# Performance work log

Hardware: AMD Instinct MI355X
Metric: run time of the kernel (lower is better)

The kernel has to match this reference:

```python
import jax, jax.numpy as jnp
import numpy as np

N_FEAT = 256
N_HID = 128
N_HEAD = 4
N_HEAD_LAST = 6
N_CLASS = 40
NEG_SLOPE = 0.2


def gat_conv(x, src, dst, W, att_src, att_dst, bias, heads, ch, concat):
    # x: [N, in], W: [in, heads*ch], att_*: [heads, ch]
    N = x.shape[0]
    xw = (x @ W).reshape(N, heads, ch)                      # [N, H, C]
    a_src = jnp.sum(xw * att_src, axis=-1)                  # [N, H]
    a_dst = jnp.sum(xw * att_dst, axis=-1)                  # [N, H]
    e = jax.nn.leaky_relu(a_src[src] + a_dst[dst], NEG_SLOPE)  # [E, H]
    # softmax over incoming edges of each destination node
    m = jax.ops.segment_max(e, dst, num_segments=N)         # [N, H]
    ex = jnp.exp(e - m[dst])
    denom = jax.ops.segment_sum(ex, dst, num_segments=N)    # [N, H]
    alpha = ex / (denom[dst] + 1e-16)                       # [E, H]
    msg = xw[src] * alpha[..., None]                        # [E, H, C]
    out = jax.ops.segment_sum(msg, dst, num_segments=N)     # [N, H, C]
    out = out.reshape(N, heads * ch) if concat else out.mean(axis=1)
    return out + bias


def setup_inputs() -> dict:
    key = jax.random.key(0)
    ks = jax.random.split(key, 16)
    N, E = 10000, 160000
    x = jax.random.normal(ks[0], (N, N_FEAT), dtype=jnp.float32)
    edge_index = jax.random.randint(ks[1], (2, E), 0, N, dtype=jnp.int64)
    hid = N_HID * N_HEAD  # 512
    s = lambda fan: 1.0 / np.sqrt(fan)
    return {
        "x": x,
        "edge_index": edge_index,
        "W0": jax.random.normal(ks[2], (N_FEAT, hid), jnp.float32) * s(N_FEAT),
        "a_src0": jax.random.normal(ks[3], (N_HEAD, N_HID), jnp.float32) * s(N_HID),
        "a_dst0": jax.random.normal(ks[4], (N_HEAD, N_HID), jnp.float32) * s(N_HID),
        "b0": jnp.zeros((hid,), jnp.float32),
        "Wskip_in": jax.random.normal(ks[5], (N_FEAT, hid), jnp.float32) * s(N_FEAT),
        "W1": jax.random.normal(ks[6], (hid, hid), jnp.float32) * s(hid),
        "a_src1": jax.random.normal(ks[7], (N_HEAD, N_HID), jnp.float32) * s(N_HID),
        "a_dst1": jax.random.normal(ks[8], (N_HEAD, N_HID), jnp.float32) * s(N_HID),
        "b1": jnp.zeros((hid,), jnp.float32),
        "W2": jax.random.normal(ks[9], (hid, N_HEAD_LAST * N_CLASS), jnp.float32) * s(hid),
        "a_src2": jax.random.normal(ks[10], (N_HEAD_LAST, N_CLASS), jnp.float32) * s(N_CLASS),
        "a_dst2": jax.random.normal(ks[11], (N_HEAD_LAST, N_CLASS), jnp.float32) * s(N_CLASS),
        "b2": jnp.zeros((N_CLASS,), jnp.float32),
        "Wskip_out": jax.random.normal(ks[12], (hid, N_CLASS), jnp.float32) * s(hid),
    }


def reference(x, edge_index, W0, a_src0, a_dst0, b0, Wskip_in,
              W1, a_src1, a_dst1, b1,
              W2, a_src2, a_dst2, b2, Wskip_out):
    N = x.shape[0]
    loops = jnp.arange(N, dtype=edge_index.dtype)
    src = jnp.concatenate([edge_index[0], loops])  # add self loops (PyG GATConv)
    dst = jnp.concatenate([edge_index[1], loops])
    # eval mode: dropout is identity
    h = gat_conv(x, src, dst, W0, a_src0, a_dst0, b0, N_HEAD, N_HID, True)
    x1 = jax.nn.elu(h + x @ Wskip_in)                      # res skip w/ projection
    h = gat_conv(x1, src, dst, W1, a_src1, a_dst1, b1, N_HEAD, N_HID, True)
    x2 = jax.nn.elu(h + x1)                                # res skip, same dims
    h = gat_conv(x2, src, dst, W2, a_src2, a_dst2, b2, N_HEAD_LAST, N_CLASS, False)
    out = h + x2 @ Wskip_out                               # out_skip 'res'
    return out
```

## Files before the change

kernel.cpp:

```cpp
#include <hip/hip_runtime.h>
#include <math.h>


#define N_FEAT 256
#define HID 512

using u16 = unsigned short;
using bf16x8 = __attribute__((ext_vector_type(8))) __bf16;
using f32x16 = __attribute__((ext_vector_type(16))) float;

__device__ inline u16 bf16_rne(float f) {
    unsigned u = __float_as_uint(f);
    return (u16)((u + 0x7fffu + ((u >> 16) & 1u)) >> 16);
}
__device__ inline float bf16_to_f32(u16 h) {
    return __uint_as_float((unsigned)h << 16);
}
__device__ inline bf16x8 ldb8(const u16* p) {
    return *reinterpret_cast<const bf16x8*>(p);
}


__global__ void init_counts(int* cursor, int N) {
    int i = blockIdx.x * blockDim.x + threadIdx.x;
    if (i < N) cursor[i] = 1;
}

__global__ void count_edges(const int* __restrict__ ei, int E, int* cursor) {
    int e = blockIdx.x * blockDim.x + threadIdx.x;
    if (e < E) atomicAdd(&cursor[ei[E + e]], 1);
}

__global__ __launch_bounds__(1024) void scan_offsets(int* cursor, int* row_off, int N) {
    __shared__ int sdata[1024];
    int tid = threadIdx.x;
    int chunk = (N + 1023) >> 10;
    int base = tid * chunk;
    int lsum = 0;
    for (int i = 0; i < chunk; i++) {
        int idx = base + i;
        if (idx < N) lsum += cursor[idx];
    }
    sdata[tid] = lsum;
    __syncthreads();
    for (int off = 1; off < 1024; off <<= 1) {
        int t = (tid >= off) ? sdata[tid - off] : 0;
        __syncthreads();
        sdata[tid] += t;
        __syncthreads();
    }
    int run = sdata[tid] - lsum;
    if (tid == 0) row_off[0] = 0;
    for (int i = 0; i < chunk; i++) {
        int idx = base + i;
        if (idx < N) {
            int c = cursor[idx];
            cursor[idx] = run;
            run += c;
            row_off[idx + 1] = run;
        }
    }
}

__global__ void fill_csr(const int* __restrict__ ei, int E, int N,
                         int* cursor, int* __restrict__ col) {
    int i = blockIdx.x * blockDim.x + threadIdx.x;
    int tot = E + N;
    if (i >= tot) return;
    int s, d;
    if (i < E) { s = ei[i]; d = ei[E + i]; }
    else       { s = i - E; d = s; }
    int pos = atomicAdd(&cursor[d], 1);
    col[pos] = s;
}


__global__ __launch_bounds__(256) void att_combine_all(
        const float* __restrict__ W0, const float* __restrict__ as0, const float* __restrict__ ad0,
        const float* __restrict__ W1, const float* __restrict__ as1, const float* __restrict__ ad1,
        const float* __restrict__ W2, const float* __restrict__ as2, const float* __restrict__ ad2,
        float* __restrict__ ac0, float* __restrict__ ac1, float* __restrict__ ac2) {
    int i = blockIdx.x * blockDim.x + threadIdx.x;
    const float *W, *as_, *ad_;
    float* ac;
    int K, H, C, li;
    if (i < 2048)       { W = W0; as_ = as0; ad_ = ad0; ac = ac0; K = 256; H = 4; C = 128; li = i; }
    else if (i < 6144)  { W = W1; as_ = as1; ad_ = ad1; ac = ac1; K = 512; H = 4; C = 128; li = i - 2048; }
    else if (i < 12288) { W = W2; as_ = as2; ad_ = ad2; ac = ac2; K = 512; H = 6; C = 40;  li = i - 6144; }
    else return;
    int k = li / (2 * H);
    int hh = li - k * 2 * H;
    int h = (hh >= H) ? hh - H : hh;
    const float* av = ((hh >= H) ? ad_ : as_) + h * C;
    const float* wp = W + (size_t)k * H * C + (size_t)h * C;
    float sum = 0.f;
    for (int c = 0; c < C; c++) sum = fmaf(wp[c], av[c], sum);
    ac[(size_t)k * 2 * H + hh] = sum;
}


__global__ __launch_bounds__(256) void cvtA_pack(const float* __restrict__ X,
                                                 u16* __restrict__ hi, u16* __restrict__ lo,
                                                 int M, int K, int Rblocks) {
    int gid = blockIdx.x * blockDim.x + threadIdx.x;
    int lane = gid & 63;
    int rest = gid >> 6;
    int KC = K >> 4;
    int R = rest / KC;
    int c = rest - R * KC;
    if (R >= Rblocks) return;
    int row = R * 32 + (lane & 31);
    if (row >= M) row = M - 1;
    const float* src = X + (size_t)row * K + c * 16 + (lane >> 5) * 8;
    float4 v0 = *reinterpret_cast<const float4*>(src);
    float4 v1 = *reinterpret_cast<const float4*>(src + 4);
    float vv[8] = {v0.x, v0.y, v0.z, v0.w, v1.x, v1.y, v1.z, v1.w};
    unsigned hp[4], lp[4];
    #pragma unroll
    for (int j = 0; j < 4; j++) {
        u16 h0 = bf16_rne(vv[2 * j]);
        u16 h1 = bf16_rne(vv[2 * j + 1]);
        float r0 = vv[2 * j]     - __uint_as_float((unsigned)h0 << 16);
        float r1 = vv[2 * j + 1] - __uint_as_float((unsigned)h1 << 16);
        u16 l0 = bf16_rne(r0);
        u16 l1 = bf16_rne(r1);
        hp[j] = (unsigned)h0 | ((unsigned)h1 << 16);
        lp[j] = (unsigned)l0 | ((unsigned)l1 << 16);
    }
    size_t dst = ((size_t)rest * 64 + lane) * 8;
    *reinterpret_cast<int4*>(hi + dst) = make_int4(hp[0], hp[1], hp[2], hp[3]);
    *reinterpret_cast<int4*>(lo + dst) = make_int4(lp[0], lp[1], lp[2], lp[3]);
}

__device__ inline void cvtB_body(const float* __restrict__ B,
                                 u16* __restrict__ hi, u16* __restrict__ lo,
                                 int K, int Nb, int gid) {
    int lane = gid & 63;
    int rest = gid >> 6;
    int KC = K >> 4;
    int Cb = rest / KC;
    int c = rest - Cb * KC;
    int n = Cb * 32 + (lane & 31);
    int kbase = c * 16 + (lane >> 5) * 8;
    float vv[8];
    #pragma unroll
    for (int j = 0; j < 8; j++)
        vv[j] = (n < Nb) ? B[(size_t)(kbase + j) * Nb + n] : 0.f;
    unsigned hp[4], lp[4];
    #pragma unroll
    for (int j = 0; j < 4; j++) {
        u16 h0 = bf16_rne(vv[2 * j]);
        u16 h1 = bf16_rne(vv[2 * j + 1]);
        float r0 = vv[2 * j]     - __uint_as_float((unsigned)h0 << 16);
        float r1 = vv[2 * j + 1] - __uint_as_float((unsigned)h1 << 16);
        u16 l0 = bf16_rne(r0);
        u16 l1 = bf16_rne(r1);
        hp[j] = (unsigned)h0 | ((unsigned)h1 << 16);
        lp[j] = (unsigned)l0 | ((unsigned)l1 << 16);
    }
    size_t dst = ((size_t)rest * 64 + lane) * 8;
    *reinterpret_cast<int4*>(hi + dst) = make_int4(hp[0], hp[1], hp[2], hp[3]);
    *reinterpret_cast<int4*>(lo + dst) = make_int4(lp[0], lp[1], lp[2], lp[3]);
}

__global__ __launch_bounds__(256) void pack_all_B(
        const float* __restrict__ W0, const float* __restrict__ Wsi, const float* __restrict__ ac0,
        const float* __restrict__ W1, const float* __restrict__ ac1,
        const float* __restrict__ W2, const float* __restrict__ Wso, const float* __restrict__ ac2,
        u16* __restrict__ B0h, u16* __restrict__ B0l,
        u16* __restrict__ B1h, u16* __restrict__ B1l,
        u16* __restrict__ B2h, u16* __restrict__ B2l) {
    int g = blockIdx.x * blockDim.x + threadIdx.x;
    if (g < 16384)      cvtB_body(W0,  B0h, B0l, 256, 512, g);
    else if (g < 32768) cvtB_body(Wsi, B0h + (size_t)16 * 16 * 512, B0l + (size_t)16 * 16 * 512, 256, 512, g - 16384);
    else if (g < 34816) cvtB_body(ac0, B0h + (size_t)32 * 16 * 512, B0l + (size_t)32 * 16 * 512, 256, 8,   g - 32768);
    else if (g < 67584) cvtB_body(W1,  B1h, B1l, 512, 512, g - 34816);
    else if (g < 71680) cvtB_body(ac1, B1h + (size_t)16 * 32 * 512, B1l + (size_t)16 * 32 * 512, 512, 8,   g - 67584);
    else if (g < 88064) cvtB_body(W2,  B2h, B2l, 512, 240, g - 71680);
    else if (g < 92160) cvtB_body(Wso, B2h + (size_t)8 * 32 * 512,  B2l + (size_t)8 * 32 * 512,  512, 40,  g - 88064);
    else if (g < 96256) cvtB_body(ac2, B2h + (size_t)10 * 32 * 512, B2l + (size_t)10 * 32 * 512, 512, 12,  g - 92160);
}


__global__ __launch_bounds__(256) void gemm_fused(const u16* __restrict__ Ahi,
                                                  const u16* __restrict__ Alo,
                                                  const u16* __restrict__ Bhi,
                                                  const u16* __restrict__ Blo,
                                                  u16* __restrict__ xwb, int xwCols,
                                                  float* __restrict__ skipP,
                                                  int skipBeg, int skipEnd,
                                                  float* __restrict__ asrc,
                                                  float* __restrict__ adst,
                                                  int attBeg, int H,
                                                  int M, int K,
                                                  int ntiles, int Rblocks) {
    int nwg = gridDim.x, b = blockIdx.x;
    int q = nwg >> 3, r = nwg & 7;
    int xcd = b & 7, idx = b >> 3;
    int t = (xcd < r) ? (xcd * (q + 1) + idx)
                      : (r * (q + 1) + (xcd - r) * q + idx);
    int bm = (t / ntiles) * 128;
    int bn = (t - (t / ntiles) * ntiles) * 64;

    int lane = threadIdx.x & 63, w = threadIdx.x >> 6;
    int wr = w >> 1, wc = w & 1;
    int l31 = lane & 31, lg = lane >> 5;
    int KC = K >> 4;

    int R0 = (bm + wr * 64) >> 5;
    int R1 = R0 + 1;
    if (R0 >= Rblocks) R0 = Rblocks - 1;
    if (R1 >= Rblocks) R1 = Rblocks - 1;
    int Cb = (bn + wc * 32) >> 5;

    const u16* pa0h = Ahi + (((size_t)R0 * KC) * 64 + lane) * 8;
    const u16* pa0l = Alo + (((size_t)R0 * KC) * 64 + lane) * 8;
    const u16* pa1h = Ahi + (((size_t)R1 * KC) * 64 + lane) * 8;
    const u16* pa1l = Alo + (((size_t)R1 * KC) * 64 + lane) * 8;
    const u16* pbh  = Bhi + (((size_t)Cb * KC) * 64 + lane) * 8;
    const u16* pbl  = Blo + (((size_t)Cb * KC) * 64 + lane) * 8;

    f32x16 acc0, acc1;
    #pragma unroll
    for (int i2 = 0; i2 < 16; i2++) { acc0[i2] = 0.f; acc1[i2] = 0.f; }

    bf16x8 a0h = ldb8(pa0h), a0l = ldb8(pa0l);
    bf16x8 a1h = ldb8(pa1h), a1l = ldb8(pa1l);
    bf16x8 bh  = ldb8(pbh),  bl  = ldb8(pbl);

    for (int c = 1; c <= KC; c++) {
        size_t off = (size_t)c * 512;
        bf16x8 na0h = ldb8(pa0h + off), na0l = ldb8(pa0l + off);
        bf16x8 na1h = ldb8(pa1h + off), na1l = ldb8(pa1l + off);
        bf16x8 nbh  = ldb8(pbh + off),  nbl  = ldb8(pbl + off);
        acc0 = __builtin_amdgcn_mfma_f32_32x32x16_bf16(a0h, bh, acc0, 0, 0, 0);
        acc1 = __builtin_amdgcn_mfma_f32_32x32x16_bf16(a1h, bh, acc1, 0, 0, 0);
        acc0 = __builtin_amdgcn_mfma_f32_32x32x16_bf16(a0h, bl, acc0, 0, 0, 0);
        acc1 = __builtin_amdgcn_mfma_f32_32x32x16_bf16(a1h, bl, acc1, 0, 0, 0);
        acc0 = __builtin_amdgcn_mfma_f32_32x32x16_bf16(a0l, bh, acc0, 0, 0, 0);
        acc1 = __builtin_amdgcn_mfma_f32_32x32x16_bf16(a1l, bh, acc1, 0, 0, 0);
        a0h = na0h; a0l = na0l; a1h = na1h; a1l = na1l; bh = nbh; bl = nbl;
    }

    int n = bn + wc * 32 + l31;
    int base_m = bm + wr * 64;
    #pragma unroll
    for (int rg = 0; rg < 16; rg++) {
        int mrow = (rg & 3) + 8 * (rg >> 2) + 4 * lg;
        int m0 = base_m + mrow;
        int m1 = m0 + 32;
        float v0 = acc0[rg], v1 = acc1[rg];
        if (n < xwCols) {
            if (m0 < M) xwb[(size_t)m0 * xwCols + n] = bf16_rne(v0);
            if (m1 < M) xwb[(size_t)m1 * xwCols + n] = bf16_rne(v1);
        } else if (n >= skipBeg && n < skipEnd) {
            int cc = n - skipBeg, st = skipEnd - skipBeg;
            if (m0 < M) skipP[(size_t)m0 * st + cc] = v0;
            if (m1 < M) skipP[(size_t)m1 * st + cc] = v1;
        } else if (n >= attBeg && n < attBeg + H) {
            int h = n - attBeg;
            if (m0 < M) asrc[(size_t)m0 * H + h] = v0;
            if (m1 < M) asrc[(size_t)m1 * H + h] = v1;
        } else if (n >= attBeg + H && n < attBeg + 2 * H) {
            int h = n - attBeg - H;
            if (m0 < M) adst[(size_t)m0 * H + h] = v0;
            if (m1 < M) adst[(size_t)m1 * H + h] = v1;
        }
    }
}


template <int SKIPPK>
__global__ __launch_bounds__(256) void agg_sm512(const u16* __restrict__ xw,
                                                 const float* __restrict__ asrc,
                                                 const float* __restrict__ adst,
                                                 const int* __restrict__ row_off,
                                                 const int* __restrict__ col,
                                                 const float* __restrict__ bias,
                                                 const float* __restrict__ skipF,
                                                 const u16* __restrict__ skipHi,
                                                 const u16* __restrict__ skipLo,
                                                 u16* __restrict__ outHi,
                                                 u16* __restrict__ outLo,
                                                 int N) {
    __shared__ float lalpha[4][256 * 4];
    __shared__ int   lcol[4][256];
    int w = (blockIdx.x * blockDim.x + threadIdx.x) >> 6;
    int lane = threadIdx.x & 63;
    int wid = (threadIdx.x >> 6) & 3;
    bool valid = w < N;
    int jb = 0, je = 0;
    float adn[4], m[4], inv[4];

    if (valid) {
        jb = row_off[w]; je = row_off[w + 1];
        float4 ad4 = *reinterpret_cast<const float4*>(&adst[(size_t)w * 4]);
        adn[0] = ad4.x; adn[1] = ad4.y; adn[2] = ad4.z; adn[3] = ad4.w;

        float ev[4][4];
        int scol[4];
        #pragma unroll
        for (int h = 0; h < 4; h++) m[h] = -INFINITY;

        #pragma unroll
        for (int c = 0; c < 4; c++) {
            int j = jb + c * 64 + lane;
            if (j < je) {
                int s = col[j]; scol[c] = s;
                float4 as4 = *reinterpret_cast<const float4*>(&asrc[(size_t)s * 4]);
                float e0 = as4.x + adn[0]; e0 = e0 > 0.f ? e0 : 0.2f * e0;
                float e1 = as4.y + adn[1]; e1 = e1 > 0.f ? e1 : 0.2f * e1;
                float e2 = as4.z + adn[2]; e2 = e2 > 0.f ? e2 : 0.2f * e2;
                float e3 = as4.w + adn[3]; e3 = e3 > 0.f ? e3 : 0.2f * e3;
                ev[c][0] = e0; ev[c][1] = e1; ev[c][2] = e2; ev[c][3] = e3;
                m[0] = fmaxf(m[0], e0); m[1] = fmaxf(m[1], e1);
                m[2] = fmaxf(m[2], e2); m[3] = fmaxf(m[3], e3);
            } else {
                scol[c] = -1;
                #pragma unroll
                for (int h = 0; h < 4; h++) ev[c][h] = -INFINITY;
            }
        }
        for (int j = jb + 256 + lane; j < je; j += 64) {
            int s = col[j];
            #pragma unroll
            for (int h = 0; h < 4; h++) {
                float e = asrc[(size_t)s * 4 + h] + adn[h];
                e = e > 0.f ? e : 0.2f * e;
                m[h] = fmaxf(m[h], e);
            }
        }
        #pragma unroll
        for (int off = 32; off; off >>= 1)
            #pragma unroll
            for (int h = 0; h < 4; h++) m[h] = fmaxf(m[h], __shfl_xor(m[h], off));

        float ssum[4] = {0.f, 0.f, 0.f, 0.f};
        #pragma unroll
        for (int c = 0; c < 4; c++)
            #pragma unroll
            for (int h = 0; h < 4; h++) ssum[h] += __expf(ev[c][h] - m[h]);
        for (int j = jb + 256 + lane; j < je; j += 64) {
            int s = col[j];
            #pragma unroll
            for (int h = 0; h < 4; h++) {
                float e = asrc[(size_t)s * 4 + h] + adn[h];
                e = e > 0.f ? e : 0.2f * e;
                ssum[h] += __expf(e - m[h]);
            }
        }
        #pragma unroll
        for (int off = 32; off; off >>= 1)
            #pragma unroll
            for (int h = 0; h < 4; h++) ssum[h] += __shfl_xor(ssum[h], off);
        #pragma unroll
        for (int h = 0; h < 4; h++) inv[h] = 1.f / (ssum[h] + 1e-16f);

        #pragma unroll
        for (int c = 0; c < 4; c++) {
            int rel = c * 64 + lane;
            if (jb + rel < je) {
                lcol[wid][rel] = scol[c];
                *reinterpret_cast<float4*>(&lalpha[wid][rel * 4]) = make_float4(
                    __expf(ev[c][0] - m[0]) * inv[0],
                    __expf(ev[c][1] - m[1]) * inv[1],
                    __expf(ev[c][2] - m[2]) * inv[2],
                    __expf(ev[c][3] - m[3]) * inv[3]);
            }
        }
    }
    __syncthreads();
    if (!valid) return;

    int base = lane * 8;
    int hme = lane >> 4;
    float acc[8] = {};
    int deg = je - jb;
    int fast = deg < 256 ? deg : 256;

    int j = 0;
    for (; j + 3 < fast; j += 4) {
        int4 cs = *reinterpret_cast<const int4*>(&lcol[wid][j]);
        float a0 = lalpha[wid][(j + 0) * 4 + hme];
        float a1 = lalpha[wid][(j + 1) * 4 + hme];
        float a2 = lalpha[wid][(j + 2) * 4 + hme];
        float a3 = lalpha[wid][(j + 3) * 4 + hme];
        uint4 r0 = *reinterpret_cast<const uint4*>(&xw[(size_t)cs.x * 512 + base]);
        uint4 r1 = *reinterpret_cast<const uint4*>(&xw[(size_t)cs.y * 512 + base]);
        uint4 r2 = *reinterpret_cast<const uint4*>(&xw[(size_t)cs.z * 512 + base]);
        uint4 r3 = *reinterpret_cast<const uint4*>(&xw[(size_t)cs.w * 512 + base]);
        acc[0] = fmaf(a0, __uint_as_float(r0.x << 16), acc[0]);
        acc[1] = fmaf(a0, __uint_as_float(r0.x & 0xffff0000u), acc[1]);
        acc[2] = fmaf(a0, __uint_as_float(r0.y << 16), acc[2]);
        acc[3] = fmaf(a0, __uint_as_float(r0.y & 0xffff0000u), acc[3]);
        acc[4] = fmaf(a0, __uint_as_float(r0.z << 16), acc[4]);
        acc[5] = fmaf(a0, __uint_as_float(r0.z & 0xffff0000u), acc[5]);
        acc[6] = fmaf(a0, __uint_as_float(r0.w << 16), acc[6]);
        acc[7] = fmaf(a0, __uint_as_float(r0.w & 0xffff0000u), acc[7]);
        acc[0] = fmaf(a1, __uint_as_float(r1.x << 16), acc[0]);
        acc[1] = fmaf(a1, __uint_as_float(r1.x & 0xffff0000u), acc[1]);
        acc[2] = fmaf(a1, __uint_as_float(r1.y << 16), acc[2]);
        acc[3] = fmaf(a1, __uint_as_float(r1.y & 0xffff0000u), acc[3]);
        acc[4] = fmaf(a1, __uint_as_float(r1.z << 16), acc[4]);
        acc[5] = fmaf(a1, __uint_as_float(r1.z & 0xffff0000u), acc[5]);
        acc[6] = fmaf(a1, __uint_as_float(r1.w << 16), acc[6]);
        acc[7] = fmaf(a1, __uint_as_float(r1.w & 0xffff0000u), acc[7]);
        acc[0] = fmaf(a2, __uint_as_float(r2.x << 16), acc[0]);
        acc[1] = fmaf(a2, __uint_as_float(r2.x & 0xffff0000u), acc[1]);
        acc[2] = fmaf(a2, __uint_as_float(r2.y << 16), acc[2]);
        acc[3] = fmaf(a2, __uint_as_float(r2.y & 0xffff0000u), acc[3]);
        acc[4] = fmaf(a2, __uint_as_float(r2.z << 16), acc[4]);
        acc[5] = fmaf(a2, __uint_as_float(r2.z & 0xffff0000u), acc[5]);
        acc[6] = fmaf(a2, __uint_as_float(r2.w << 16), acc[6]);
        acc[7] = fmaf(a2, __uint_as_float(r2.w & 0xffff0000u), acc[7]);
        acc[0] = fmaf(a3, __uint_as_float(r3.x << 16), acc[0]);
        acc[1] = fmaf(a3, __uint_as_float(r3.x & 0xffff0000u), acc[1]);
        acc[2] = fmaf(a3, __uint_as_float(r3.y << 16), acc[2]);
        acc[3] = fmaf(a3, __uint_as_float(r3.y & 0xffff0000u), acc[3]);
        acc[4] = fmaf(a3, __uint_as_float(r3.z << 16), acc[4]);
        acc[5] = fmaf(a3, __uint_as_float(r3.z & 0xffff0000u), acc[5]);
        acc[6] = fmaf(a3, __uint_as_float(r3.w << 16), acc[6]);
        acc[7] = fmaf(a3, __uint_as_float(r3.w & 0xffff0000u), acc[7]);
    }
    for (; j < fast; ++j) {
        int s = lcol[wid][j];
        float a = lalpha[wid][j * 4 + hme];
        uint4 raw = *reinterpret_cast<const uint4*>(&xw[(size_t)s * 512 + base]);
        acc[0] = fmaf(a, __uint_as_float(raw.x << 16), acc[0]);
        acc[1] = fmaf(a, __uint_as_float(raw.x & 0xffff0000u), acc[1]);
        acc[2] = fmaf(a, __uint_as_float(raw.y << 16), acc[2]);
        acc[3] = fmaf(a, __uint_as_float(raw.y & 0xffff0000u), acc[3]);
        acc[4] = fmaf(a, __uint_as_float(raw.z << 16), acc[4]);
        acc[5] = fmaf(a, __uint_as_float(raw.z & 0xffff0000u), acc[5]);
        acc[6] = fmaf(a, __uint_as_float(raw.w << 16), acc[6]);
        acc[7] = fmaf(a, __uint_as_float(raw.w & 0xffff0000u), acc[7]);
    }
    if (deg > 256) {
        float adn_h = hme == 0 ? adn[0] : hme == 1 ? adn[1] : hme == 2 ? adn[2] : adn[3];
        float m_h   = hme == 0 ? m[0]   : hme == 1 ? m[1]   : hme == 2 ? m[2]   : m[3];
        float inv_h = hme == 0 ? inv[0] : hme == 1 ? inv[1] : hme == 2 ? inv[2] : inv[3];
        for (int jj = jb + 256; jj < je; ++jj) {
            int s = col[jj];
            float e = asrc[(size_t)s * 4 + hme] + adn_h;
            e = e > 0.f ? e : 0.2f * e;
            float a = __expf(e - m_h) * inv_h;
            uint4 raw = *reinterpret_cast<const uint4*>(&xw[(size_t)s * 512 + base]);
            acc[0] = fmaf(a, __uint_as_float(raw.x << 16), acc[0]);
            acc[1] = fmaf(a, __uint_as_float(raw.x & 0xffff0000u), acc[1]);
            acc[2] = fmaf(a, __uint_as_float(raw.y << 16), acc[2]);
            acc[3] = fmaf(a, __uint_as_float(raw.y & 0xffff0000u), acc[3]);
            acc[4] = fmaf(a, __uint_as_float(raw.z << 16), acc[4]);
            acc[5] = fmaf(a, __uint_as_float(raw.z & 0xffff0000u), acc[5]);
            acc[6] = fmaf(a, __uint_as_float(raw.w << 16), acc[6]);
            acc[7] = fmaf(a, __uint_as_float(raw.w & 0xffff0000u), acc[7]);
        }
    }

    int R = w >> 5, r31 = w & 31, cc = lane >> 1, sub = lane & 1;
    int lp = r31 | (sub << 5);
    size_t slot = (((size_t)R * 32 + cc) * 64 + lp) * 8;

    float sk[8];
    if (SKIPPK) {
        int4 h4 = *reinterpret_cast<const int4*>(skipHi + slot);
        int4 l4 = *reinterpret_cast<const int4*>(skipLo + slot);
        unsigned hu[4] = {(unsigned)h4.x, (unsigned)h4.y, (unsigned)h4.z, (unsigned)h4.w};
        unsigned lu[4] = {(unsigned)l4.x, (unsigned)l4.y, (unsigned)l4.z, (unsigned)l4.w};
        #pragma unroll
        for (int i = 0; i < 4; i++) {
            sk[2 * i]     = __uint_as_float(hu[i] << 16) + __uint_as_float(lu[i] << 16);
            sk[2 * i + 1] = __uint_as_float(hu[i] & 0xffff0000u)
                          + __uint_as_float(lu[i] & 0xffff0000u);
        }
    } else {
        const float* kp = &skipF[(size_t)w * 512 + base];
        float4 s0 = *reinterpret_cast<const float4*>(kp);
        float4 s1 = *reinterpret_cast<const float4*>(kp + 4);
        sk[0] = s0.x; sk[1] = s0.y; sk[2] = s0.z; sk[3] = s0.w;
        sk[4] = s1.x; sk[5] = s1.y; sk[6] = s1.z; sk[7] = s1.w;
    }

    const float* bp = &bias[base];
    float r[8];
    #pragma unroll
    for (int i = 0; i < 8; i++) {
        float v = acc[i] + bp[i] + sk[i];
        r[i] = v > 0.f ? v : expm1f(v);
    }

    unsigned hp[4], lpk[4];
    #pragma unroll
    for (int i = 0; i < 4; i++) {
        u16 h0 = bf16_rne(r[2 * i]);
        u16 h1 = bf16_rne(r[2 * i + 1]);
        float q0 = r[2 * i]     - __uint_as_float((unsigned)h0 << 16);
        float q1 = r[2 * i + 1] - __uint_as_float((unsigned)h1 << 16);
        u16 l0 = bf16_rne(q0);
        u16 l1 = bf16_rne(q1);
        hp[i]  = (unsigned)h0 | ((unsigned)h1 << 16);
        lpk[i] = (unsigned)l0 | ((unsigned)l1 << 16);
    }
    *reinterpret_cast<int4*>(outHi + slot) = make_int4(hp[0], hp[1], hp[2], hp[3]);
    *reinterpret_cast<int4*>(outLo + slot) = make_int4(lpk[0], lpk[1], lpk[2], lpk[3]);
}


__global__ __launch_bounds__(256) void agg_final240_sm(const u16* __restrict__ xw,
                                                       const float* __restrict__ asrc,
                                                       const float* __restrict__ adst,
                                                       const int* __restrict__ row_off,
                                                       const int* __restrict__ col,
                                                       const float* __restrict__ b2,
                                                       const float* __restrict__ skip,
                                                       float* __restrict__ out,
                                                       int N) {
    __shared__ float lalpha[4][256 * 6];
    __shared__ int   lcol[4][256];
    int w = (blockIdx.x * blockDim.x + threadIdx.x) >> 6;
    int lane = threadIdx.x & 63;
    int wid = (threadIdx.x >> 6) & 3;
    bool valid = w < N;
    int jb = 0, je = 0;
    float adn[6], m[6], inv[6];

    if (valid) {
        jb = row_off[w]; je = row_off[w + 1];
        #pragma unroll
        for (int h = 0; h < 6; h++) adn[h] = adst[(size_t)w * 6 + h];

        float ev[4][6];
        int scol[4];
        #pragma unroll
        for (int h = 0; h < 6; h++) m[h] = -INFINITY;

        #pragma unroll
        for (int c = 0; c < 4; c++) {
            int j = jb + c * 64 + lane;
            if (j < je) {
                int s = col[j]; scol[c] = s;
                #pragma unroll
                for (int h = 0; h < 6; h++) {
                    float e = asrc[(size_t)s * 6 + h] + adn[h];
                    e = e > 0.f ? e : 0.2f * e;
                    ev[c][h] = e;
                    m[h] = fmaxf(m[h], e);
                }
            } else {
                scol[c] = -1;
                #pragma unroll
                for (int h = 0; h < 6; h++) ev[c][h] = -INFINITY;
            }
        }
        for (int j = jb + 256 + lane; j < je; j += 64) {
            int s = col[j];
            #pragma unroll
            for (int h = 0; h < 6; h++) {
                float e = asrc[(size_t)s * 6 + h] + adn[h];
                e = e > 0.f ? e : 0.2f * e;
                m[h] = fmaxf(m[h], e);
            }
        }
        #pragma unroll
        for (int off = 32; off; off >>= 1)
            #pragma unroll
            for (int h = 0; h < 6; h++) m[h] = fmaxf(m[h], __shfl_xor(m[h], off));

        float ssum[6] = {0.f, 0.f, 0.f, 0.f, 0.f, 0.f};
        #pragma unroll
        for (int c = 0; c < 4; c++)
            #pragma unroll
            for (int h = 0; h < 6; h++) ssum[h] += __expf(ev[c][h] - m[h]);
        for (int j = jb + 256 + lane; j < je; j += 64) {
            int s = col[j];
            #pragma unroll
            for (int h = 0; h < 6; h++) {
                float e = asrc[(size_t)s * 6 + h] + adn[h];
                e = e > 0.f ? e : 0.2f * e;
                ssum[h] += __expf(e - m[h]);
            }
        }
        #pragma unroll
        for (int off = 32; off; off >>= 1)
            #pragma unroll
            for (int h = 0; h < 6; h++) ssum[h] += __shfl_xor(ssum[h], off);
        #pragma unroll
        for (int h = 0; h < 6; h++) inv[h] = 1.f / (ssum[h] + 1e-16f);

        #pragma unroll
        for (int c = 0; c < 4; c++) {
            int rel = c * 64 + lane;
            if (jb + rel < je) {
                lcol[wid][rel] = scol[c];
                #pragma unroll
                for (int h = 0; h < 6; h++)
                    lalpha[wid][rel * 6 + h] = __expf(ev[c][h] - m[h]) * inv[h];
            }
        }
    }
    __syncthreads();
    if (!valid) return;

    bool active = lane < 40;
    float acc[6] = {};
    int deg = je - jb;
    int fast = deg < 256 ? deg : 256;

    int j = 0;
    for (; j + 1 < fast; j += 2) {
        int s0 = lcol[wid][j], s1 = lcol[wid][j + 1];
        const float* ap0 = &lalpha[wid][j * 6];
        const float* ap1 = &lalpha[wid][(j + 1) * 6];
        if (active) {
            const u16* sp0 = &xw[(size_t)s0 * 240 + lane];
            const u16* sp1 = &xw[(size_t)s1 * 240 + lane];
            #pragma unroll
            for (int h = 0; h < 6; h++) {
                acc[h] = fmaf(ap0[h], bf16_to_f32(sp0[h * 40]), acc[h]);
                acc[h] = fmaf(ap1[h], bf16_to_f32(sp1[h * 40]), acc[h]);
            }
        }
    }
    for (; j < fast; ++j) {
        int s = lcol[wid][j];
        const float* ap = &lalpha[wid][j * 6];
        if (active) {
            const u16* sp = &xw[(size_t)s * 240 + lane];
            #pragma unroll
            for (int h = 0; h < 6; h++)
                acc[h] = fmaf(ap[h], bf16_to_f32(sp[h * 40]), acc[h]);
        }
    }
    if (deg > 256) {
        for (int jj = jb + 256; jj < je; ++jj) {
            int s = col[jj];
            if (active) {
                const u16* sp = &xw[(size_t)s * 240 + lane];
                #pragma unroll
                for (int h = 0; h < 6; h++) {
                    float e = asrc[(size_t)s * 6 + h] + adn[h];
                    e = e > 0.f ? e : 0.2f * e;
                    float a = __expf(e - m[h]) * inv[h];
                    acc[h] = fmaf(a, bf16_to_f32(sp[h * 40]), acc[h]);
                }
            }
        }
    }
    if (active) {
        float v = (acc[0] + acc[1] + acc[2] + acc[3] + acc[4] + acc[5]) * (1.f / 6.f)
                  + b2[lane] + skip[(size_t)w * 40 + lane];
        out[(size_t)w * 40 + lane] = v;
    }
}


extern "C" void kernel_launch(void* const* d_in, const int* in_sizes, int n_in,
                              void* d_out, int out_size, void* d_ws, size_t ws_size,
                              hipStream_t stream) {
    const float* x        = (const float*)d_in[0];
    const int*   ei       = (const int*)  d_in[1];
    const float* W0       = (const float*)d_in[2];
    const float* a_src0   = (const float*)d_in[3];
    const float* a_dst0   = (const float*)d_in[4];
    const float* b0       = (const float*)d_in[5];
    const float* Wskip_in = (const float*)d_in[6];
    const float* W1       = (const float*)d_in[7];
    const float* a_src1   = (const float*)d_in[8];
    const float* a_dst1   = (const float*)d_in[9];
    const float* b1       = (const float*)d_in[10];
    const float* W2       = (const float*)d_in[11];
    const float* a_src2   = (const float*)d_in[12];
    const float* a_dst2   = (const float*)d_in[13];
    const float* b2       = (const float*)d_in[14];
    const float* Wskip_out= (const float*)d_in[15];

    const int N = in_sizes[0] / N_FEAT;
    const int E = in_sizes[1] / 2;
    float* out = (float*)d_out;

    const int Rblocks = (N + 31) / 32;
    const int mtiles = (N + 127) / 128;

    float* ws = (float*)d_ws;
    size_t o = 0;
    u16* xwb   = (u16*)(ws + o); o += (size_t)N * 256;
    float* tmpD  = ws + o; o += (size_t)N * HID;
    float* asrc  = ws + o; o += (size_t)N * 8;
    float* adst  = ws + o; o += (size_t)N * 8;
    float* skipo = ws + o; o += (size_t)N * 40;
    float* ac0   = ws + o; o += 256 * 8;
    float* ac1   = ws + o; o += 512 * 8;
    float* ac2   = ws + o; o += 512 * 12;

    u16* up = (u16*)(ws + o);
    size_t uo = 0;
    const size_t aPack = (size_t)Rblocks * 32 * 512 + 512;
    u16* AhA = up + uo; uo += aPack;   u16* AlA = up + uo; uo += aPack;
    u16* AhB = up + uo; uo += aPack;   u16* AlB = up + uo; uo += aPack;
    const size_t b0sz = (size_t)34 * 16 * 512 + 512;
    u16* B0h = up + uo; uo += b0sz;  u16* B0l = up + uo; uo += b0sz;
    const size_t b1sz = (size_t)18 * 32 * 512 + 512;
    u16* B1h = up + uo; uo += b1sz;  u16* B1l = up + uo; uo += b1sz;
    const size_t b2sz = (size_t)12 * 32 * 512 + 512;
    u16* B2h = up + uo; uo += b2sz;  u16* B2l = up + uo; uo += b2sz;
    int* row_off = (int*)(up + uo);
    int* cursor  = row_off + (N + 1);
    int* col     = cursor + (N + 1);

    init_counts<<<(N + 255) / 256, 256, 0, stream>>>(cursor, N);
    count_edges<<<(E + 255) / 256, 256, 0, stream>>>(ei, E, cursor);
    scan_offsets<<<1, 1024, 0, stream>>>(cursor, row_off, N);
    fill_csr<<<(E + N + 255) / 256, 256, 0, stream>>>(ei, E, N, cursor, col);

    att_combine_all<<<48, 256, 0, stream>>>(W0, a_src0, a_dst0,
                                            W1, a_src1, a_dst1,
                                            W2, a_src2, a_dst2, ac0, ac1, ac2);
    pack_all_B<<<376, 256, 0, stream>>>(W0, Wskip_in, ac0, W1, ac1,
                                        W2, Wskip_out, ac2,
                                        B0h, B0l, B1h, B1l, B2h, B2l);

    int nodeBlocks = (N * 64 + 255) / 256;
    const int BIG = 1 << 30;

    cvtA_pack<<<(Rblocks * 16 * 64 + 255) / 256, 256, 0, stream>>>(x, AhA, AlA, N, 256, Rblocks);
    gemm_fused<<<mtiles * 17, 256, 0, stream>>>(
        AhA, AlA, B0h, B0l, xwb, 512, tmpD, 512, 1024, asrc, adst, 1024, 4,
        N, 256, 17, Rblocks);
    agg_sm512<0><<<nodeBlocks, 256, 0, stream>>>(
        xwb, asrc, adst, row_off, col, b0, tmpD, nullptr, nullptr, AhB, AlB, N);

    gemm_fused<<<mtiles * 9, 256, 0, stream>>>(
        AhB, AlB, B1h, B1l, xwb, 512, nullptr, BIG, BIG, asrc, adst, 512, 4,
        N, 512, 9, Rblocks);
    agg_sm512<1><<<nodeBlocks, 256, 0, stream>>>(
        xwb, asrc, adst, row_off, col, b1, nullptr, AhB, AlB, AhA, AlA, N);

    gemm_fused<<<mtiles * 6, 256, 0, stream>>>(
        AhA, AlA, B2h, B2l, xwb, 240, skipo, 256, 296, asrc, adst, 320, 6,
        N, 512, 6, Rblocks);
    agg_final240_sm<<<nodeBlocks, 256, 0, stream>>>(
        xwb, asrc, adst, row_off, col, b2, skipo, out, N);
}
```

Before: 343.4 us.

## Split each node's aggregation across two waves and vectorize final-layer gathers

The 512-wide aggregation kernel now gives each destination node two wavefronts that process alternating edges, then merges their partial sums through shared memory. The block covers two nodes instead of four, so the grid doubles and more loads are in flight for each node. The final 240-wide aggregation is reworked so 60 lanes each gather four contiguous bf16 values with 8-byte loads, in place of 40 lanes doing six scalar loads each. Partial head sums are then combined through shared memory. Both changes add an extra barrier and shared-memory traffic, and the 512-wide kernel repeats the softmax setup in both waves.

```diff
diff --git a/kernel.cpp b/kernel.cpp
--- a/kernel.cpp
+++ b/kernel.cpp
@@ -18,6 +18,16 @@
 }
 __device__ inline bf16x8 ldb8(const u16* p) {
     return *reinterpret_cast<const bf16x8*>(p);
+}
+__device__ inline void acc8(float a, const uint4 r, float* acc) {
+    acc[0] = fmaf(a, __uint_as_float(r.x << 16), acc[0]);
+    acc[1] = fmaf(a, __uint_as_float(r.x & 0xffff0000u), acc[1]);
+    acc[2] = fmaf(a, __uint_as_float(r.y << 16), acc[2]);
+    acc[3] = fmaf(a, __uint_as_float(r.y & 0xffff0000u), acc[3]);
+    acc[4] = fmaf(a, __uint_as_float(r.z << 16), acc[4]);
+    acc[5] = fmaf(a, __uint_as_float(r.z & 0xffff0000u), acc[5]);
+    acc[6] = fmaf(a, __uint_as_float(r.w << 16), acc[6]);
+    acc[7] = fmaf(a, __uint_as_float(r.w & 0xffff0000u), acc[7]);
 }
 
 
@@ -283,11 +293,15 @@
                                                  u16* __restrict__ outHi,
                                                  u16* __restrict__ outLo,
                                                  int N) {
-    __shared__ float lalpha[4][256 * 4];
-    __shared__ int   lcol[4][256];
-    int w = (blockIdx.x * blockDim.x + threadIdx.x) >> 6;
-    int lane = threadIdx.x & 63;
-    int wid = (threadIdx.x >> 6) & 3;
+    __shared__ float lalpha[2][256 * 4];
+    __shared__ int   lcol[2][256];
+    __shared__ float lmerge[2][512];
+    int tid = threadIdx.x;
+    int widx = tid >> 6;
+    int p = widx >> 1;
+    int half = widx & 1;
+    int lane = tid & 63;
+    int w = blockIdx.x * 2 + p;
     bool valid = w < N;
     int jb = 0, je = 0;
     float adn[4], m[4], inv[4];
@@ -360,8 +374,8 @@
         for (int c = 0; c < 4; c++) {
             int rel = c * 64 + lane;
             if (jb + rel < je) {
-                lcol[wid][rel] = scol[c];
-                *reinterpret_cast<float4*>(&lalpha[wid][rel * 4]) = make_float4(
+                lcol[p][rel] = scol[c];
+                *reinterpret_cast<float4*>(&lalpha[p][rel * 4]) = make_float4(
                     __expf(ev[c][0] - m[0]) * inv[0],
                     __expf(ev[c][1] - m[1]) * inv[1],
                     __expf(ev[c][2] - m[2]) * inv[2],
@@ -370,7 +384,6 @@
         }
     }
     __syncthreads();
-    if (!valid) return;
 
     int base = lane * 8;
     int hme = lane >> 4;
@@ -378,82 +391,51 @@
     int deg = je - jb;
     int fast = deg < 256 ? deg : 256;
 
-    int j = 0;
-    for (; j + 3 < fast; j += 4) {
-        int4 cs = *reinterpret_cast<const int4*>(&lcol[wid][j]);
-        float a0 = lalpha[wid][(j + 0) * 4 + hme];
-        float a1 = lalpha[wid][(j + 1) * 4 + hme];
-        float a2 = lalpha[wid][(j + 2) * 4 + hme];
-        float a3 = lalpha[wid][(j + 3) * 4 + hme];
-        uint4 r0 = *reinterpret_cast<const uint4*>(&xw[(size_t)cs.x * 512 + base]);
-        uint4 r1 = *reinterpret_cast<const uint4*>(&xw[(size_t)cs.y * 512 + base]);
-        uint4 r2 = *reinterpret_cast<const uint4*>(&xw[(size_t)cs.z * 512 + base]);
-        uint4 r3 = *reinterpret_cast<const uint4*>(&xw[(size_t)cs.w * 512 + base]);
-        acc[0] = fmaf(a0, __uint_as_float(r0.x << 16), acc[0]);
-        acc[1] = fmaf(a0, __uint_as_float(r0.x & 0xffff0000u), acc[1]);
-        acc[2] = fmaf(a0, __uint_as_float(r0.y << 16), acc[2]);
-        acc[3] = fmaf(a0, __uint_as_float(r0.y & 0xffff0000u), acc[3]);
-        acc[4] = fmaf(a0, __uint_as_float(r0.z << 16), acc[4]);
-        acc[5] = fmaf(a0, __uint_as_float(r0.z & 0xffff0000u), acc[5]);
-        acc[6] = fmaf(a0, __uint_as_float(r0.w << 16), acc[6]);
-        acc[7] = fmaf(a0, __uint_as_float(r0.w & 0xffff0000u), acc[7]);
-        acc[0] = fmaf(a1, __uint_as_float(r1.x << 16), acc[0]);
-        acc[1] = fmaf(a1, __uint_as_float(r1.x & 0xffff0000u), acc[1]);
-        acc[2] = fmaf(a1, __uint_as_float(r1.y << 16), acc[2]);
-        acc[3] = fmaf(a1, __uint_as_float(r1.y & 0xffff0000u), acc[3]);
-        acc[4] = fmaf(a1, __uint_as_float(r1.z << 16), acc[4]);
-        acc[5] = fmaf(a1, __uint_as_float(r1.z & 0xffff0000u), acc[5]);
-        acc[6] = fmaf(a1, __uint_as_float(r1.w << 16), acc[6]);
-        acc[7] = fmaf(a1, __uint_as_float(r1.w & 0xffff0000u), acc[7]);
-        acc[0] = fmaf(a2, __uint_as_float(r2.x << 16), acc[0]);
-        acc[1] = fmaf(a2, __uint_as_float(r2.x & 0xffff0000u), acc[1]);
-        acc[2] = fmaf(a2, __uint_as_float(r2.y << 16), acc[2]);
-        acc[3] = fmaf(a2, __uint_as_float(r2.y & 0xffff0000u), acc[3]);
-        acc[4] = fmaf(a2, __uint_as_float(r2.z << 16), acc[4]);
-        acc[5] = fmaf(a2, __uint_as_float(r2.z & 0xffff0000u), acc[5]);
-        acc[6] = fmaf(a2, __uint_as_float(r2.w << 16), acc[6]);
-        acc[7] = fmaf(a2, __uint_as_float(r2.w & 0xffff0000u), acc[7]);
-        acc[0] = fmaf(a3, __uint_as_float(r3.x << 16), acc[0]);
-        acc[1] = fmaf(a3, __uint_as_float(r3.x & 0xffff0000u), acc[1]);
-        acc[2] = fmaf(a3, __uint_as_float(r3.y << 16), acc[2]);
-        acc[3] = fmaf(a3, __uint_as_float(r3.y & 0xffff0000u), acc[3]);
-        acc[4] = fmaf(a3, __uint_as_float(r3.z << 16), acc[4]);
-        acc[5] = fmaf(a3, __uint_as_float(r3.z & 0xffff0000u), acc[5]);
-        acc[6] = fmaf(a3, __uint_as_float(r3.w << 16), acc[6]);
-        acc[7] = fmaf(a3, __uint_as_float(r3.w & 0xffff0000u), acc[7]);
-    }
-    for (; j < fast; ++j) {
-        int s = lcol[wid][j];
-        float a = lalpha[wid][j * 4 + hme];
-        uint4 raw = *reinterpret_cast<const uint4*>(&xw[(size_t)s * 512 + base]);
-        acc[0] = fmaf(a, __uint_as_float(raw.x << 16), acc[0]);
-        acc[1] = fmaf(a, __uint_as_float(raw.x & 0xffff0000u), acc[1]);
-        acc[2] = fmaf(a, __uint_as_float(raw.y << 16), acc[2]);
-        acc[3] = fmaf(a, __uint_as_float(raw.y & 0xffff0000u), acc[3]);
-        acc[4] = fmaf(a, __uint_as_float(raw.z << 16), acc[4]);
-        acc[5] = fmaf(a, __uint_as_float(raw.z & 0xffff0000u), acc[5]);
-        acc[6] = fmaf(a, __uint_as_float(raw.w << 16), acc[6]);
-        acc[7] = fmaf(a, __uint_as_float(raw.w & 0xffff0000u), acc[7]);
-    }
-    if (deg > 256) {
-        float adn_h = hme == 0 ? adn[0] : hme == 1 ? adn[1] : hme == 2 ? adn[2] : adn[3];
-        float m_h   = hme == 0 ? m[0]   : hme == 1 ? m[1]   : hme == 2 ? m[2]   : m[3];
-        float inv_h = hme == 0 ? inv[0] : hme == 1 ? inv[1] : hme == 2 ? inv[2] : inv[3];
-        for (int jj = jb + 256; jj < je; ++jj) {
-            int s = col[jj];
-            float e = asrc[(size_t)s * 4 + hme] + adn_h;
-            e = e > 0.f ? e : 0.2f * e;
-            float a = __expf(e - m_h) * inv_h;
+    if (valid) {
+        int j = half;
+        for (; j + 6 < fast; j += 8) {
+            int s0 = lcol[p][j],     s1 = lcol[p][j + 2];
+            int s2 = lcol[p][j + 4], s3 = lcol[p][j + 6];
+            float a0 = lalpha[p][(j + 0) * 4 + hme];
+            float a1 = lalpha[p][(j + 2) * 4 + hme];
+            float a2 = lalpha[p][(j + 4) * 4 + hme];
+            float a3 = lalpha[p][(j + 6) * 4 + hme];
+            uint4 r0 = *reinterpret_cast<const uint4*>(&xw[(size_t)s0 * 512 + base]);
+            uint4 r1 = *reinterpret_cast<const uint4*>(&xw[(size_t)s1 * 512 + base]);
+            uint4 r2 = *reinterpret_cast<const uint4*>(&xw[(size_t)s2 * 512 + base]);
+            uint4 r3 = *reinterpret_cast<const uint4*>(&xw[(size_t)s3 * 512 + base]);
+            acc8(a0, r0, acc); acc8(a1, r1, acc);
+            acc8(a2, r2, acc); acc8(a3, r3, acc);
+        }
+        for (; j < fast; j += 2) {
+            int s = lcol[p][j];
+            float a = lalpha[p][j * 4 + hme];
             uint4 raw = *reinterpret_cast<const uint4*>(&xw[(size_t)s * 512 + base]);
-            acc[0] = fmaf(a, __uint_as_float(raw.x << 16), acc[0]);
-            acc[1] = fmaf(a, __uint_as_float(raw.x & 0xffff0000u), acc[1]);
-            acc[2] = fmaf(a, __uint_as_float(raw.y << 16), acc[2]);
-            acc[3] = fmaf(a, __uint_as_float(raw.y & 0xffff0000u), acc[3]);
-            acc[4] = fmaf(a, __uint_as_float(raw.z << 16), acc[4]);
-            acc[5] = fmaf(a, __uint_as_float(raw.z & 0xffff0000u), acc[5]);
-            acc[6] = fmaf(a, __uint_as_float(raw.w << 16), acc[6]);
-            acc[7] = fmaf(a, __uint_as_float(raw.w & 0xffff0000u), acc[7]);
-        }
+            acc8(a, raw, acc);
+        }
+        if (deg > 256 && half == 0) {
+            for (int jj = jb + 256; jj < je; ++jj) {
+                int s = col[jj];
+                float e = asrc[(size_t)s * 4 + hme] + adn[hme];
+                e = e > 0.f ? e : 0.2f * e;
+                float a = __expf(e - m[hme]) * inv[hme];
+                uint4 raw = *reinterpret_cast<const uint4*>(&xw[(size_t)s * 512 + base]);
+                acc8(a, raw, acc);
+            }
+        }
+        if (half == 1) {
+            *reinterpret_cast<float4*>(&lmerge[p][base])     = make_float4(acc[0], acc[1], acc[2], acc[3]);
+            *reinterpret_cast<float4*>(&lmerge[p][base + 4]) = make_float4(acc[4], acc[5], acc[6], acc[7]);
+        }
+    }
+    __syncthreads();
+    if (!valid || half == 1) return;
+
+    {
+        float4 m0 = *reinterpret_cast<const float4*>(&lmerge[p][base]);
+        float4 m1 = *reinterpret_cast<const float4*>(&lmerge[p][base + 4]);
+        acc[0] += m0.x; acc[1] += m0.y; acc[2] += m0.z; acc[3] += m0.w;
+        acc[4] += m1.x; acc[5] += m1.y; acc[6] += m1.z; acc[7] += m1.w;
     }
 
     int R = w >> 5, r31 = w & 31, cc = lane >> 1, sub = lane & 1;
@@ -516,6 +498,7 @@
                                                        int N) {
     __shared__ float lalpha[4][256 * 6];
     __shared__ int   lcol[4][256];
+    __shared__ float lmerge[4][240];
     int w = (blockIdx.x * blockDim.x + threadIdx.x) >> 6;
     int lane = threadIdx.x & 63;
     int wid = (threadIdx.x >> 6) & 3;
@@ -598,56 +581,78 @@
         }
     }
     __syncthreads();
-    if (!valid) return;
-
-    bool active = lane < 40;
-    float acc[6] = {};
+
+    int h60 = lane / 10;
+    int i10 = lane - h60 * 10;
+    bool activeB = lane < 60;
+    int coff = h60 * 40 + i10 * 4;
+    float acc[4] = {};
     int deg = je - jb;
     int fast = deg < 256 ? deg : 256;
 
-    int j = 0;
-    for (; j + 1 < fast; j += 2) {
-        int s0 = lcol[wid][j], s1 = lcol[wid][j + 1];
-        const float* ap0 = &lalpha[wid][j * 6];
-        const float* ap1 = &lalpha[wid][(j + 1) * 6];
-        if (active) {
-            const u16* sp0 = &xw[(size_t)s0 * 240 + lane];
-            const u16* sp1 = &xw[(size_t)s1 * 240 + lane];
-            #pragma unroll
-            for (int h = 0; h < 6; h++) {
-                acc[h] = fmaf(ap0[h], bf16_to_f32(sp0[h * 40]), acc[h]);
-                acc[h] = fmaf(ap1[h], bf16_to_f32(sp1[h * 40]), acc[h]);
-            }
-        }
-    }
-    for (; j < fast; ++j) {
-        int s = lcol[wid][j];
-        const float* ap = &lalpha[wid][j * 6];
-        if (active) {
-            const u16* sp = &xw[(size_t)s * 240 + lane];
-            #pragma unroll
-            for (int h = 0; h < 6; h++)
-                acc[h] = fmaf(ap[h], bf16_to_f32(sp[h * 40]), acc[h]);
-        }
-    }
-    if (deg > 256) {
-        for (int jj = jb + 256; jj < je; ++jj) {
-            int s = col[jj];
-            if (active) {
-                const u16* sp = &xw[(size_t)s * 240 + lane];
-                #pragma unroll
-                for (int h = 0; h < 6; h++) {
-                    float e = asrc[(size_t)s * 6 + h] + adn[h];
-                    e = e > 0.f ? e : 0.2f * e;
-                    float a = __expf(e - m[h]) * inv[h];
-                    acc[h] = fmaf(a, bf16_to_f32(sp[h * 40]), acc[h]);
-                }
-            }
-        }
-    }
-    if (active) {
-        float v = (acc[0] + acc[1] + acc[2] + acc[3] + acc[4] + acc[5]) * (1.f / 6.f)
-                  + b2[lane] + skip[(size_t)w * 40 + lane];
+    if (valid && activeB) {
+        int j = 0;
+        for (; j + 3 < fast; j += 4) {
+            int s0 = lcol[wid][j],     s1 = lcol[wid][j + 1];
+            int s2 = lcol[wid][j + 2], s3 = lcol[wid][j + 3];
+            float a0 = lalpha[wid][(j + 0) * 6 + h60];
+            float a1 = lalpha[wid][(j + 1) * 6 + h60];
+            float a2 = lalpha[wid][(j + 2) * 6 + h60];
+            float a3 = lalpha[wid][(j + 3) * 6 + h60];
+            uint2 r0 = *reinterpret_cast<const uint2*>(&xw[(size_t)s0 * 240 + coff]);
+            uint2 r1 = *reinterpret_cast<const uint2*>(&xw[(size_t)s1 * 240 + coff]);
+            uint2 r2 = *reinterpret_cast<const uint2*>(&xw[(size_t)s2 * 240 + coff]);
+            uint2 r3 = *reinterpret_cast<const uint2*>(&xw[(size_t)s3 * 240 + coff]);
+            acc[0] = fmaf(a0, __uint_as_float(r0.x << 16), acc[0]);
+            acc[1] = fmaf(a0, __uint_as_float(r0.x & 0xffff0000u), acc[1]);
+            acc[2] = fmaf(a0, __uint_as_float(r0.y << 16), acc[2]);
+            acc[3] = fmaf(a0, __uint_as_float(r0.y & 0xffff0000u), acc[3]);
+            acc[0] = fmaf(a1, __uint_as_float(r1.x << 16), acc[0]);
+            acc[1] = fmaf(a1, __uint_as_float(r1.x & 0xffff0000u), acc[1]);
+            acc[2] = fmaf(a1, __uint_as_float(r1.y << 16), acc[2]);
+            acc[3] = fmaf(a1, __uint_as_float(r1.y & 0xffff0000u), acc[3]);
+            acc[0] = fmaf(a2, __uint_as_float(r2.x << 16), acc[0]);
+            acc[1] = fmaf(a2, __uint_as_float(r2.x & 0xffff0000u), acc[1]);
+            acc[2] = fmaf(a2, __uint_as_float(r2.y << 16), acc[2]);
+            acc[3] = fmaf(a2, __uint_as_float(r2.y & 0xffff0000u), acc[3]);
+            acc[0] = fmaf(a3, __uint_as_float(r3.x << 16), acc[0]);
+            acc[1] = fmaf(a3, __uint_as_float(r3.x & 0xffff0000u), acc[1]);
+            acc[2] = fmaf(a3, __uint_as_float(r3.y << 16), acc[2]);
+            acc[3] = fmaf(a3, __uint_as_float(r3.y & 0xffff0000u), acc[3]);
+        }
+        for (; j < fast; ++j) {
+            int s = lcol[wid][j];
+            float a = lalpha[wid][j * 6 + h60];
+            uint2 raw = *reinterpret_cast<const uint2*>(&xw[(size_t)s * 240 + coff]);
+            acc[0] = fmaf(a, __uint_as_float(raw.x << 16), acc[0]);
+            acc[1] = fmaf(a, __uint_as_float(raw.x & 0xffff0000u), acc[1]);
+            acc[2] = fmaf(a, __uint_as_float(raw.y << 16), acc[2]);
+            acc[3] = fmaf(a, __uint_as_float(raw.y & 0xffff0000u), acc[3]);
+        }
+        if (deg > 256) {
+            for (int jj = jb + 256; jj < je; ++jj) {
+                int s = col[jj];
+                float e = asrc[(size_t)s * 6 + h60] + adn[h60];
+                e = e > 0.f ? e : 0.2f * e;
+                float a = __expf(e - m[h60]) * inv[h60];
+                uint2 raw = *reinterpret_cast<const uint2*>(&xw[(size_t)s * 240 + coff]);
+                acc[0] = fmaf(a, __uint_as_float(raw.x << 16), acc[0]);
+                acc[1] = fmaf(a, __uint_as_float(raw.x & 0xffff0000u), acc[1]);
+                acc[2] = fmaf(a, __uint_as_float(raw.y << 16), acc[2]);
+                acc[3] = fmaf(a, __uint_as_float(raw.y & 0xffff0000u), acc[3]);
+            }
+        }
+        *reinterpret_cast<float4*>(&lmerge[wid][lane * 4]) =
+            make_float4(acc[0], acc[1], acc[2], acc[3]);
+    }
+    __syncthreads();
+    if (!valid) return;
+
+    if (lane < 40) {
+        float s = 0.f;
+        #pragma unroll
+        for (int h = 0; h < 6; h++) s += lmerge[wid][h * 40 + lane];
+        float v = s * (1.f / 6.f) + b2[lane] + skip[(size_t)w * 40 + lane];
         out[(size_t)w * 40 + lane] = v;
     }
 }
@@ -718,6 +723,7 @@
                                         W2, Wskip_out, ac2,
                                         B0h, B0l, B1h, B1l, B2h, B2l);
 
+    int pairBlocks = (N + 1) / 2;
     int nodeBlocks = (N * 64 + 255) / 256;
     const int BIG = 1 << 30;
 
@@ -725,13 +731,13 @@
     gemm_fused<<<mtiles * 17, 256, 0, stream>>>(
         AhA, AlA, B0h, B0l, xwb, 512, tmpD, 512, 1024, asrc, adst, 1024, 4,
         N, 256, 17, Rblocks);
-    agg_sm512<0><<<nodeBlocks, 256, 0, stream>>>(
+    agg_sm512<0><<<pairBlocks, 256, 0, stream>>>(
         xwb, asrc, adst, row_off, col, b0, tmpD, nullptr, nullptr, AhB, AlB, N);
 
     gemm_fused<<<mtiles * 9, 256, 0, stream>>>(
         AhB, AlB, B1h, B1l, xwb, 512, nullptr, BIG, BIG, asrc, adst, 512, 4,
         N, 512, 9, Rblocks);
-    agg_sm512<1><<<nodeBlocks, 256, 0, stream>>>(
+    agg_sm512<1><<<pairBlocks, 256, 0, stream>>>(
         xwb, asrc, adst, row_off, col, b1, nullptr, AhB, AlB, AhA, AlA, N);
 
     gemm_fused<<<mtiles * 6, 256, 0, stream>>>(
```

After: 345.7 us. Within noise of the previous version (+0.7%).
